# Performance work log

Measured on AMD Instinct MI355X. Metric: run time of the kernel, lower is better.

The kernel has to match this reference:

```python
import math
import jax, jax.numpy as jnp
import numpy as np


def _gelu(x):
    return jax.nn.gelu(x, approximate=False)


def _bilinear_sample(feat, gx, gy):
    """grid_sample, mode=bilinear, padding=border, align_corners=True.
    feat: [B,C,H,W]; gx,gy: [B,M] in [-1,1]. Returns [B,M,C]."""
    B, C, H, W = feat.shape
    x = jnp.clip((gx + 1.0) * 0.5 * (W - 1), 0.0, W - 1)
    y = jnp.clip((gy + 1.0) * 0.5 * (H - 1), 0.0, H - 1)
    x0 = jnp.floor(x); y0 = jnp.floor(y)
    wx = (x - x0)[..., None]; wy = (y - y0)[..., None]
    x0i = x0.astype(jnp.int32); y0i = y0.astype(jnp.int32)
    x1i = jnp.minimum(x0i + 1, W - 1); y1i = jnp.minimum(y0i + 1, H - 1)
    ft = jnp.transpose(feat, (0, 2, 3, 1))  # [B,H,W,C]
    gather = jax.vmap(lambda f, yi, xi: f[yi, xi])
    v00 = gather(ft, y0i, x0i); v01 = gather(ft, y0i, x1i)
    v10 = gather(ft, y1i, x0i); v11 = gather(ft, y1i, x1i)
    return (v00 * (1 - wx) * (1 - wy) + v01 * wx * (1 - wy)
            + v10 * (1 - wx) * wy + v11 * wx * wy)


def _layernorm(x, w, b, eps=1e-5):
    m = jnp.mean(x, -1, keepdims=True)
    v = jnp.var(x, -1, keepdims=True)
    return (x - m) / jnp.sqrt(v + eps) * w + b


def _gfb(h, f_next, ph_w, ph_b, gate, w1, b1, w2, b2, ln_w, ln_b):
    g = jax.nn.sigmoid(gate)
    fused = f_next + g * (h @ ph_w + ph_b)
    fused = _gelu(fused @ w1 + b1) @ w2 + b2
    return _layernorm(fused, ln_w, ln_b)


def _forward(img, feat_s8, feat_s16, coarse_flow, query_coords,
             pp_w1, pp_b1, pp_w2, pp_b2, p8_w, p8_b, p16_w, p16_b,
             f1_ph_w, f1_ph_b, f1_gate, f1_w1, f1_b1, f1_w2, f1_b2, f1_ln_w, f1_ln_b,
             f2_ph_w, f2_ph_b, f2_gate, f2_w1, f2_b1, f2_w2, f2_b2, f2_ln_w, f2_ln_b,
             h_w1, h_b1, h_w2, h_b2, h_w3, h_b3):
    B, _, H, W = img.shape
    N = query_coords.shape[1]
    k = 5; half = k // 2
    H8, W8 = coarse_flow.shape[2], coarse_flow.shape[3]
    # normalized grid at query points (x,y)
    gx = 2.0 * query_coords[..., 0] / (W - 1) - 1.0
    gy = 2.0 * query_coords[..., 1] / (H - 1) - 1.0
    coarse_q = _bilinear_sample(coarse_flow, gx, gy)  # [B,N,2]
    coarse_q = coarse_q * jnp.array([W / W8, H / H8], coarse_q.dtype)
    # local k x k RGB patches
    offs = jnp.arange(-half, half + 1, dtype=img.dtype)
    oy, ox = jnp.meshgrid(offs, offs, indexing='ij')
    og = jnp.stack([ox.reshape(-1), oy.reshape(-1)], -1)  # [k*k,2]
    ce = query_coords[:, :, None, :] + og                # [B,N,kk,2]
    pgx = (2.0 * ce[..., 0] / (W - 1) - 1.0).reshape(B, -1)
    pgy = (2.0 * ce[..., 1] / (H - 1) - 1.0).reshape(B, -1)
    patches = _bilinear_sample(img, pgx, pgy).reshape(B, N, k * k * 3)
    f_local = _gelu(patches @ pp_w1 + pp_b1) @ pp_w2 + pp_b2
    f8 = _bilinear_sample(feat_s8, gx, gy) @ p8_w + p8_b
    f16 = _bilinear_sample(feat_s16, gx, gy) @ p16_w + p16_b
    D = f_local.shape[-1]
    h = f_local.reshape(B * N, D)
    h = _gfb(h, f8.reshape(B * N, D), f1_ph_w, f1_ph_b, f1_gate,
             f1_w1, f1_b1, f1_w2, f1_b2, f1_ln_w, f1_ln_b)
    h = _gfb(h, f16.reshape(B * N, D), f2_ph_w, f2_ph_b, f2_gate,
             f2_w1, f2_b1, f2_w2, f2_b2, f2_ln_w, f2_ln_b)
    # relative-in-cell coords + sinusoidal PE (6 bands)
    qx = query_coords[..., 0] / (W / W8)
    qy = query_coords[..., 1] / (H / H8)
    local = jnp.stack([(qx - jnp.round(qx)) * 2.0, (qy - jnp.round(qy)) * 2.0], -1)
    freqs = (2.0 ** jnp.arange(6, dtype=local.dtype)) * math.pi
    xf = local[..., None] * freqs                        # [B,N,2,6]
    enc = jnp.concatenate([jnp.sin(xf), jnp.cos(xf)], -1).reshape(B, N, 24)
    pe = jnp.concatenate([local, enc], -1).reshape(B * N, 26)
    coarse_flat = coarse_q.reshape(B * N, 2)
    mi = jnp.concatenate([h, pe, coarse_flat], -1)       # [B*N, 156]
    delta = _gelu(_gelu(mi @ h_w1 + h_b1) @ h_w2 + h_b2) @ h_w3 + h_b3
    return (coarse_flat + delta).reshape(B, N, 2)


def setup_inputs() -> dict:
    key = jax.random.key(0)
    ks = jax.random.split(key, 40)
    B, H, W = 2, 384, 512
    H8, W8, H16, W16 = 48, 64, 24, 32
    N, D, k = 65536, 128, 5
    pf = 3 * k * k
    def p(i, shape):
        return jax.random.normal(ks[i], shape, jnp.float32) * 0.05
    return {
        'img': jax.random.uniform(ks[0], (B, 3, H, W), jnp.float32),
        'feat_s8': jax.random.normal(ks[1], (B, D, H8, W8), jnp.float32),
        'feat_s16': jax.random.normal(ks[2], (B, D, H16, W16), jnp.float32),
        'coarse_flow': jax.random.normal(ks[3], (B, 2, H8, W8), jnp.float32),
        'query_coords': jax.random.uniform(ks[4], (B, N, 2), jnp.float32)
                        * jnp.array([W - 1.0, H - 1.0], jnp.float32),
        'pp_w1': p(5, (pf, D)), 'pp_b1': p(6, (D,)),
        'pp_w2': p(7, (D, D)), 'pp_b2': p(8, (D,)),
        'p8_w': p(9, (D, D)), 'p8_b': p(10, (D,)),
        'p16_w': p(11, (D, D)), 'p16_b': p(12, (D,)),
        'f1_ph_w': p(13, (D, D)), 'f1_ph_b': p(14, (D,)), 'f1_gate': p(15, (D,)),
        'f1_w1': p(16, (D, 2 * D)), 'f1_b1': p(17, (2 * D,)),
        'f1_w2': p(18, (2 * D, D)), 'f1_b2': p(19, (D,)),
        'f1_ln_w': 1.0 + p(20, (D,)), 'f1_ln_b': p(21, (D,)),
        'f2_ph_w': p(22, (D, D)), 'f2_ph_b': p(23, (D,)), 'f2_gate': p(24, (D,)),
        'f2_w1': p(25, (D, 2 * D)), 'f2_b1': p(26, (2 * D,)),
        'f2_w2': p(27, (2 * D, D)), 'f2_b2': p(28, (D,)),
        'f2_ln_w': 1.0 + p(29, (D,)), 'f2_ln_b': p(30, (D,)),
        'h_w1': p(31, (D + 26 + 2, 128)), 'h_b1': p(32, (128,)),
        'h_w2': p(33, (128, 64)), 'h_b2': p(34, (64,)),
        'h_w3': p(35, (64, 2)), 'h_b3': p(36, (2,)),
    }


def reference(img, feat_s8, feat_s16, coarse_flow, query_coords,
              pp_w1, pp_b1, pp_w2, pp_b2, p8_w, p8_b, p16_w, p16_b,
              f1_ph_w, f1_ph_b, f1_gate, f1_w1, f1_b1, f1_w2, f1_b2, f1_ln_w, f1_ln_b,
              f2_ph_w, f2_ph_b, f2_gate, f2_w1, f2_b1, f2_w2, f2_b2, f2_ln_w, f2_ln_b,
              h_w1, h_b1, h_w2, h_b2, h_w3, h_b3):
    return _forward(img, feat_s8, feat_s16, coarse_flow, query_coords,
                    pp_w1, pp_b1, pp_w2, pp_b2, p8_w, p8_b, p16_w, p16_b,
                    f1_ph_w, f1_ph_b, f1_gate, f1_w1, f1_b1, f1_w2, f1_b2, f1_ln_w, f1_ln_b,
                    f2_ph_w, f2_ph_b, f2_gate, f2_w1, f2_b1, f2_w2, f2_b2, f2_ln_w, f2_ln_b,
                    h_w1, h_b1, h_w2, h_b2, h_w3, h_b3)
```

## Files before the change

kernel.cpp:

```cpp
#include <hip/hip_runtime.h>
#include <math.h>

#define NT 256
#define MB 32
#define MTOT 131072
#define IMG_H 384
#define IMG_W 512
#define H8 48
#define W8 64
#define H16 24
#define W16 32

typedef _Float16 half8_t __attribute__((ext_vector_type(8)));
typedef float f32x4_t __attribute__((ext_vector_type(4)));
typedef unsigned short u16;

#define PW_PP1   0
#define PW_PP2   12288
#define PW_P8    28672
#define PW_P16   45056
#define PW_F1PH  61440
#define PW_F1W1  77824
#define PW_F1W2  110592
#define PW_F2PH  143360
#define PW_F2W1  159744
#define PW_F2W2  192512
#define PW_HW1   225280
#define PW_HW2   245760
#define PW_END   253952
#define FT8_OFF  PW_END
#define FT8_CNT  (2*H8*W8*128)
#define FT16_OFF (FT8_OFF + FT8_CNT)

__device__ __forceinline__ u16 tohalf(float v) {
  return __builtin_bit_cast(u16, (_Float16)v);
}
__device__ __forceinline__ float geluf(float x) {
  float x2 = x * x;
  float t = x * fmaf(x2, 0.0713548162726f, 1.5957691216057308f);
  float e = __expf(-t);
  return x * __builtin_amdgcn_rcpf(1.0f + e);
}
__device__ __forceinline__ float sigm(float x) {
  return __builtin_amdgcn_rcpf(1.0f + __expf(-x));
}

__device__ __forceinline__ float bilin_plane(const float* __restrict__ plane,
                                             int Wd, int Hd, float x, float y) {
  x = fminf(fmaxf(x, 0.f), (float)(Wd - 1));
  y = fminf(fmaxf(y, 0.f), (float)(Hd - 1));
  float x0f = floorf(x), y0f = floorf(y);
  int x0 = (int)x0f, y0 = (int)y0f;
  int x1 = min(x0 + 1, Wd - 1), y1 = min(y0 + 1, Hd - 1);
  float wx = x - x0f, wy = y - y0f;
  const float* r0 = plane + y0 * Wd;
  const float* r1 = plane + y1 * Wd;
  float v00 = r0[x0], v01 = r0[x1], v10 = r1[x0], v11 = r1[x1];
  float top = v00 + wx * (v01 - v00);
  float bot = v10 + wx * (v11 - v10);
  return top + wy * (bot - top);
}

__device__ __forceinline__ void featSample(const u16* __restrict__ ft, int Wd, int Hd,
                                           float x, float y, u16* dstRow, int i16) {
  x = fminf(fmaxf(x, 0.f), (float)(Wd - 1));
  y = fminf(fmaxf(y, 0.f), (float)(Hd - 1));
  float x0f = floorf(x), y0f = floorf(y);
  int x0 = (int)x0f, y0 = (int)y0f;
  int x1 = min(x0 + 1, Wd - 1), y1 = min(y0 + 1, Hd - 1);
  float wx = x - x0f, wy = y - y0f;
  half8_t v00 = *reinterpret_cast<const half8_t*>(ft + (y0 * Wd + x0) * 128 + i16 * 8);
  half8_t v01 = *reinterpret_cast<const half8_t*>(ft + (y0 * Wd + x1) * 128 + i16 * 8);
  half8_t v10 = *reinterpret_cast<const half8_t*>(ft + (y1 * Wd + x0) * 128 + i16 * 8);
  half8_t v11 = *reinterpret_cast<const half8_t*>(ft + (y1 * Wd + x1) * 128 + i16 * 8);
  half8_t r;
#pragma unroll
  for (int j = 0; j < 8; ++j) {
    float top = (float)v00[j] + wx * ((float)v01[j] - (float)v00[j]);
    float bot = (float)v10[j] + wx * ((float)v11[j] - (float)v10[j]);
    r[j] = (_Float16)(top + wy * (bot - top));
  }
  *reinterpret_cast<half8_t*>(dstRow + i16 * 8) = r;
}

template <int NTW, int KT, int SPLITKT, int ACT>
__device__ __forceinline__ void mmv(
    const u16* __restrict__ wpk,
    const u16* aA, int strA, const u16* aB, int strB,
    const float* __restrict__ bias, const float* __restrict__ gate,
    u16* oA, int ostrA, u16* oB, int ostrB, int oSplitNt) {
  const int tid = threadIdx.x;
  const int lane = tid & 63;
  const int w = tid >> 6;
  const int l15 = lane & 15;
  const int g = lane >> 4;
  f32x4_t acc[NTW][2];
#pragma unroll
  for (int i = 0; i < NTW; ++i) {
    acc[i][0] = (f32x4_t){0.f, 0.f, 0.f, 0.f};
    acc[i][1] = (f32x4_t){0.f, 0.f, 0.f, 0.f};
  }
#pragma unroll
  for (int kt = 0; kt < KT; ++kt) {
    const u16* ab = (kt < SPLITKT) ? (aA + kt * 32) : (aB + (kt - SPLITKT) * 32);
    const int str = (kt < SPLITKT) ? strA : strB;
    half8_t af0 = *reinterpret_cast<const half8_t*>(ab + l15 * str + g * 8);
    half8_t af1 = *reinterpret_cast<const half8_t*>(ab + (16 + l15) * str + g * 8);
#pragma unroll
    for (int i = 0; i < NTW; ++i) {
      const int nt = w + (i << 2);
      half8_t bf = *reinterpret_cast<const half8_t*>(wpk + ((nt * KT + kt) * 64 + lane) * 8);
      acc[i][0] = __builtin_amdgcn_mfma_f32_16x16x32_f16(af0, bf, acc[i][0], 0, 0, 0);
      acc[i][1] = __builtin_amdgcn_mfma_f32_16x16x32_f16(af1, bf, acc[i][1], 0, 0, 0);
    }
  }
#pragma unroll
  for (int i = 0; i < NTW; ++i) {
    const int nt = w + (i << 2);
    const int colg = (nt << 4) + l15;
    float bv = bias[colg];
    float sg = 0.f;
    if (ACT == 2) sg = sigm(gate[colg]);
    u16* ob; int colB, ostr;
    if (nt < oSplitNt) { ob = oA; colB = colg; ostr = ostrA; }
    else { ob = oB; colB = colg - (oSplitNt << 4); ostr = ostrB; }
#pragma unroll
    for (int mt = 0; mt < 2; ++mt) {
#pragma unroll
      for (int r = 0; r < 4; ++r) {
        const int row = (mt << 4) + (g << 2) + r;
        float v = acc[i][mt][r] + bv;
        if (ACT == 1) v = geluf(v);
        if (ACT == 2) {
          _Float16 old = __builtin_bit_cast(_Float16, ob[row * ostr + colB]);
          v = (float)old + sg * v;
        }
        ob[row * ostr + colB] = tohalf(v);
      }
    }
  }
}

__device__ __forceinline__ void lnorm(const u16* src, u16* dst,
                                      const float* __restrict__ lw,
                                      const float* __restrict__ lb) {
  const int tid = threadIdx.x;
  int q = tid >> 3, s = tid & 7;
  const u16* rp = src + q * 136 + s * 16;
  float xs[16];
  float sum = 0.f, sum2 = 0.f;
#pragma unroll
  for (int c8 = 0; c8 < 2; ++c8) {
    half8_t v = *reinterpret_cast<const half8_t*>(rp + c8 * 8);
#pragma unroll
    for (int j = 0; j < 8; ++j) {
      float x = (float)v[j];
      xs[c8 * 8 + j] = x; sum += x; sum2 += x * x;
    }
  }
  sum += __shfl_xor(sum, 1); sum2 += __shfl_xor(sum2, 1);
  sum += __shfl_xor(sum, 2); sum2 += __shfl_xor(sum2, 2);
  sum += __shfl_xor(sum, 4); sum2 += __shfl_xor(sum2, 4);
  float mean = sum * 0.0078125f;
  float var = sum2 * 0.0078125f - mean * mean;
  float rstd = rsqrtf(var + 1e-5f);
  u16* op = dst + q * 168 + s * 16;
#pragma unroll
  for (int c8 = 0; c8 < 2; ++c8) {
    half8_t r;
#pragma unroll
    for (int j = 0; j < 8; ++j) {
      int c = s * 16 + c8 * 8 + j;
      r[j] = (_Float16)((xs[c8 * 8 + j] - mean) * rstd * lw[c] + lb[c]);
    }
    *reinterpret_cast<half8_t*>(op + c8 * 8) = r;
  }
}

struct PackArgs { const float* src[12]; u16* dst; };

__global__ void pack_weights(PackArgs a) {
  const int KTs[12]   = {3, 4, 4, 4, 4, 4, 8, 4, 4, 8, 5, 4};
  const int Ks[12]    = {75, 128, 128, 128, 128, 128, 256, 128, 128, 256, 156, 128};
  const int Ns[12]    = {128, 128, 128, 128, 128, 256, 128, 128, 256, 128, 128, 64};
  const int bases[13] = {0, 12288, 28672, 45056, 61440, 77824, 110592, 143360,
                         159744, 192512, 225280, 245760, 253952};
  int stride = gridDim.x * blockDim.x;
  for (int i = blockIdx.x * blockDim.x + threadIdx.x; i < PW_END; i += stride) {
    int s = 0;
    while (i >= bases[s + 1]) ++s;
    int rem = i - bases[s];
    int e = rem & 511, lane = e >> 3, j = e & 7;
    int ntkt = rem >> 9;
    int kt = ntkt % KTs[s], nt = ntkt / KTs[s];
    int k = kt * 32 + ((lane >> 4) << 3) + j;
    int col = (nt << 4) + (lane & 15);
    float v = (k < Ks[s]) ? a.src[s][k * Ns[s] + col] : 0.f;
    a.dst[i] = tohalf(v);
  }
}

__global__ void cvt_cl_f16(const float* __restrict__ src, u16* __restrict__ dst,
                           int Hd, int Wd) {
  int total = 2 * 128 * Hd * Wd;
  int stride = gridDim.x * blockDim.x;
  for (int i = blockIdx.x * blockDim.x + threadIdx.x; i < total; i += stride) {
    int x = i % Wd;
    int t = i / Wd;
    int y = t % Hd; t /= Hd;
    int c = t % 128;
    int b = t / 128;
    dst[((b * Hd + y) * Wd + x) * 128 + c] = tohalf(src[i]);
  }
}

struct KParams {
  const float *img, *coarse_flow, *qc;
  const u16 *wpk, *ft8, *ft16;
  const float *pp_b1, *pp_b2, *p8_b, *p16_b;
  const float *f1_ph_b, *f1_gate, *f1_b1, *f1_b2, *f1_ln_w, *f1_ln_b;
  const float *f2_ph_b, *f2_gate, *f2_b1, *f2_b2, *f2_ln_w, *f2_ln_b;
  const float *h_b1, *h_b2, *h_w3, *h_b3;
  float* out;
};

__global__ __launch_bounds__(NT, 4) void ifd_mfma(KParams P) {
  __shared__ __align__(16) u16 smem[14080];
  __shared__ float qcL[64];
  __shared__ float cb[64];
  u16* ab0 = smem;
  u16* ab1 = smem + 4352;
  u16* hb  = smem + 8704;

  const int tid = threadIdx.x;
  const int m0 = blockIdx.x * MB;

  if (tid < 64) qcL[tid] = P.qc[m0 * 2 + tid];
  __syncthreads();

  for (int i = tid; i < MB * 96; i += NT) {
    int q = i / 96, c = i - q * 96;
    u16 val = 0;
    if (c < 75) {
      int m = m0 + q, b = m >> 16;
      float qx = qcL[2 * q], qy = qcL[2 * q + 1];
      int p = c / 3, ch = c - p * 3;
      int iy = p / 5, ix = p - iy * 5;
      const float* plane = P.img + (b * 3 + ch) * (IMG_H * IMG_W);
      val = tohalf(bilin_plane(plane, IMG_W, IMG_H,
                               qx + (float)(ix - 2), qy + (float)(iy - 2)));
    }
    ab0[q * 136 + c] = val;
  }
  for (int i = tid; i < MB * 40; i += NT) {
    int q = i / 40, c = i - q * 40;
    int m = m0 + q, b = m >> 16;
    float qx = qcL[2 * q], qy = qcL[2 * q + 1];
    float val = 0.f;
    if (c < 26) {
      float qx8 = qx * 0.125f, qy8 = qy * 0.125f;
      float lx = (qx8 - rintf(qx8)) * 2.f, ly = (qy8 - rintf(qy8)) * 2.f;
      if (c < 2) val = c ? ly : lx;
      else {
        int k = c - 2;
        int dim = k / 12, tt = k - dim * 12;
        int band = tt % 6, iscos = tt / 6;
        float loc = dim ? ly : lx;
        float ang = loc * 3.14159265358979323846f * (float)(1 << band);
        val = iscos ? __cosf(ang) : __sinf(ang);
      }
    } else if (c < 28) {
      int o = c - 26;
      float x8 = qx * (63.f / 511.f), y8 = qy * (47.f / 383.f);
      float cv = 8.f * bilin_plane(P.coarse_flow + (b * 2 + o) * (H8 * W8), W8, H8, x8, y8);
      cb[q * 2 + o] = cv;
      val = cv;
    }
    hb[q * 168 + 128 + c] = tohalf(val);
  }
  __syncthreads();

  mmv<2, 3, 3, 1>(P.wpk + PW_PP1, ab0, 136, ab0, 136, P.pp_b1, nullptr,
                  ab1, 136, ab1, 136, 16);
  __syncthreads();
  mmv<2, 4, 4, 0>(P.wpk + PW_PP2, ab1, 136, ab1, 136, P.pp_b2, nullptr,
                  hb, 168, hb, 168, 16);
  for (int i = tid; i < MB * 16; i += NT) {
    int q = i >> 4, i16 = i & 15;
    int m = m0 + q, b = m >> 16;
    float x = qcL[2 * q] * (63.f / 511.f), y = qcL[2 * q + 1] * (47.f / 383.f);
    featSample(P.ft8 + b * (H8 * W8 * 128), W8, H8, x, y, ab0 + q * 136, i16);
  }
  __syncthreads();
  mmv<2, 4, 4, 0>(P.wpk + PW_P8, ab0, 136, ab0, 136, P.p8_b, nullptr,
                  ab1, 136, ab1, 136, 16);
  __syncthreads();
  mmv<2, 4, 4, 2>(P.wpk + PW_F1PH, hb, 168, hb, 168, P.f1_ph_b, P.f1_gate,
                  ab1, 136, ab1, 136, 16);
  __syncthreads();
  mmv<4, 4, 4, 1>(P.wpk + PW_F1W1, ab1, 136, ab1, 136, P.f1_b1, nullptr,
                  ab0, 136, hb, 168, 8);
  __syncthreads();
  mmv<2, 8, 4, 0>(P.wpk + PW_F1W2, ab0, 136, hb, 168, P.f1_b2, nullptr,
                  ab1, 136, ab1, 136, 16);
  __syncthreads();
  lnorm(ab1, hb, P.f1_ln_w, P.f1_ln_b);
  for (int i = tid; i < MB * 16; i += NT) {
    int q = i >> 4, i16 = i & 15;
    int m = m0 + q, b = m >> 16;
    float x = qcL[2 * q] * (31.f / 511.f), y = qcL[2 * q + 1] * (23.f / 383.f);
    featSample(P.ft16 + b * (H16 * W16 * 128), W16, H16, x, y, ab0 + q * 136, i16);
  }
  __syncthreads();
  mmv<2, 4, 4, 0>(P.wpk + PW_P16, ab0, 136, ab0, 136, P.p16_b, nullptr,
                  ab1, 136, ab1, 136, 16);
  __syncthreads();
  mmv<2, 4, 4, 2>(P.wpk + PW_F2PH, hb, 168, hb, 168, P.f2_ph_b, P.f2_gate,
                  ab1, 136, ab1, 136, 16);
  __syncthreads();
  mmv<4, 4, 4, 1>(P.wpk + PW_F2W1, ab1, 136, ab1, 136, P.f2_b1, nullptr,
                  ab0, 136, hb, 168, 8);
  __syncthreads();
  mmv<2, 8, 4, 0>(P.wpk + PW_F2W2, ab0, 136, hb, 168, P.f2_b2, nullptr,
                  ab1, 136, ab1, 136, 16);
  __syncthreads();
  lnorm(ab1, hb, P.f2_ln_w, P.f2_ln_b);
  __syncthreads();
  mmv<2, 5, 5, 1>(P.wpk + PW_HW1, hb, 168, hb, 168, P.h_b1, nullptr,
                  ab1, 136, ab1, 136, 16);
  __syncthreads();
  mmv<1, 4, 4, 1>(P.wpk + PW_HW2, ab1, 136, ab1, 136, P.h_b2, nullptr,
                  ab0, 136, ab0, 136, 16);
  __syncthreads();
  if (tid < 64) {
    int q = tid >> 1, o = tid & 1;
    float acc = P.h_b3[o];
    const u16* rp = ab0 + q * 136;
#pragma unroll
    for (int c8 = 0; c8 < 8; ++c8) {
      half8_t v = *reinterpret_cast<const half8_t*>(rp + c8 * 8);
#pragma unroll
      for (int j = 0; j < 8; ++j) acc += (float)v[j] * P.h_w3[(c8 * 8 + j) * 2 + o];
    }
    P.out[(m0 + q) * 2 + o] = cb[q * 2 + o] + acc;
  }
}

extern "C" void kernel_launch(void* const* d_in, const int* in_sizes, int n_in,
                              void* d_out, int out_size, void* d_ws, size_t ws_size,
                              hipStream_t stream) {
  u16* wp = (u16*)d_ws;

  PackArgs pa;
  pa.src[0]  = (const float*)d_in[5];
  pa.src[1]  = (const float*)d_in[7];
  pa.src[2]  = (const float*)d_in[9];
  pa.src[3]  = (const float*)d_in[11];
  pa.src[4]  = (const float*)d_in[13];
  pa.src[5]  = (const float*)d_in[16];
  pa.src[6]  = (const float*)d_in[18];
  pa.src[7]  = (const float*)d_in[22];
  pa.src[8]  = (const float*)d_in[25];
  pa.src[9]  = (const float*)d_in[27];
  pa.src[10] = (const float*)d_in[31];
  pa.src[11] = (const float*)d_in[33];
  pa.dst = wp;
  pack_weights<<<512, 256, 0, stream>>>(pa);
  cvt_cl_f16<<<1024, 256, 0, stream>>>((const float*)d_in[1], wp + FT8_OFF, H8, W8);
  cvt_cl_f16<<<256, 256, 0, stream>>>((const float*)d_in[2], wp + FT16_OFF, H16, W16);

  KParams P;
  P.img = (const float*)d_in[0];
  P.coarse_flow = (const float*)d_in[3];
  P.qc = (const float*)d_in[4];
  P.wpk = wp; P.ft8 = wp + FT8_OFF; P.ft16 = wp + FT16_OFF;
  P.pp_b1 = (const float*)d_in[6];  P.pp_b2 = (const float*)d_in[8];
  P.p8_b = (const float*)d_in[10];  P.p16_b = (const float*)d_in[12];
  P.f1_ph_b = (const float*)d_in[14]; P.f1_gate = (const float*)d_in[15];
  P.f1_b1 = (const float*)d_in[17]; P.f1_b2 = (const float*)d_in[19];
  P.f1_ln_w = (const float*)d_in[20]; P.f1_ln_b = (const float*)d_in[21];
  P.f2_ph_b = (const float*)d_in[23]; P.f2_gate = (const float*)d_in[24];
  P.f2_b1 = (const float*)d_in[26]; P.f2_b2 = (const float*)d_in[28];
  P.f2_ln_w = (const float*)d_in[29]; P.f2_ln_b = (const float*)d_in[30];
  P.h_b1 = (const float*)d_in[32]; P.h_b2 = (const float*)d_in[34];
  P.h_w3 = (const float*)d_in[35]; P.h_b3 = (const float*)d_in[36];
  P.out = (float*)d_out;

  ifd_mfma<<<MTOT / MB, NT, 0, stream>>>(P);
}
```

Baseline: 205.1 us.

## Fold gated projections into concatenated-K GEMMs and vectorize MFMA epilogue stores

The sigmoid gate and the two projection matmuls per fusion block are folded algebraically into one K=256 GEMM over the concatenated [feat, h] inputs, with the gated bias precomputed by a small kernel. This removes two GEMM stages, two barriers and the read-modify-write epilogue. The MFMA operands are swapped so each lane holds four consecutive output columns, which allows half4 stores and vector bias loads. Launch bounds are raised to 5 blocks per CU, which may cause register spills.

```diff
diff --git a/kernel.cpp b/kernel.cpp
--- a/kernel.cpp
+++ b/kernel.cpp
@@ -12,25 +12,26 @@
 #define W16 32
 
 typedef _Float16 half8_t __attribute__((ext_vector_type(8)));
+typedef _Float16 half4_t __attribute__((ext_vector_type(4)));
 typedef float f32x4_t __attribute__((ext_vector_type(4)));
 typedef unsigned short u16;
 
-#define PW_PP1   0
-#define PW_PP2   12288
-#define PW_P8    28672
-#define PW_P16   45056
-#define PW_F1PH  61440
-#define PW_F1W1  77824
-#define PW_F1W2  110592
-#define PW_F2PH  143360
-#define PW_F2W1  159744
-#define PW_F2W2  192512
-#define PW_HW1   225280
-#define PW_HW2   245760
-#define PW_END   253952
-#define FT8_OFF  PW_END
-#define FT8_CNT  (2*H8*W8*128)
-#define FT16_OFF (FT8_OFF + FT8_CNT)
+#define PW_PP1    0
+#define PW_PP2    12288
+#define PW_P8CAT  28672
+#define PW_P16CAT 61440
+#define PW_F1W1   94208
+#define PW_F1W2   126976
+#define PW_F2W1   159744
+#define PW_F2W2   192512
+#define PW_HW1    225280
+#define PW_HW2    245760
+#define PW_END    253952
+#define FT8_OFF   PW_END
+#define FT8_CNT   (2*H8*W8*128)
+#define FT16_OFF  (FT8_OFF + FT8_CNT)
+#define FT16_CNT  (2*H16*W16*128)
+#define FB_OFF    (FT16_OFF + FT16_CNT)
 
 __device__ __forceinline__ u16 tohalf(float v) {
   return __builtin_bit_cast(u16, (_Float16)v);
@@ -40,9 +41,6 @@
   float t = x * fmaf(x2, 0.0713548162726f, 1.5957691216057308f);
   float e = __expf(-t);
   return x * __builtin_amdgcn_rcpf(1.0f + e);
-}
-__device__ __forceinline__ float sigm(float x) {
-  return __builtin_amdgcn_rcpf(1.0f + __expf(-x));
 }
 
 __device__ __forceinline__ float bilin_plane(const float* __restrict__ plane,
@@ -87,7 +85,7 @@
 __device__ __forceinline__ void mmv(
     const u16* __restrict__ wpk,
     const u16* aA, int strA, const u16* aB, int strB,
-    const float* __restrict__ bias, const float* __restrict__ gate,
+    const float* __restrict__ bias,
     u16* oA, int ostrA, u16* oB, int ostrB, int oSplitNt) {
   const int tid = threadIdx.x;
   const int lane = tid & 63;
@@ -110,33 +108,29 @@
     for (int i = 0; i < NTW; ++i) {
       const int nt = w + (i << 2);
       half8_t bf = *reinterpret_cast<const half8_t*>(wpk + ((nt * KT + kt) * 64 + lane) * 8);
-      acc[i][0] = __builtin_amdgcn_mfma_f32_16x16x32_f16(af0, bf, acc[i][0], 0, 0, 0);
-      acc[i][1] = __builtin_amdgcn_mfma_f32_16x16x32_f16(af1, bf, acc[i][1], 0, 0, 0);
+      acc[i][0] = __builtin_amdgcn_mfma_f32_16x16x32_f16(bf, af0, acc[i][0], 0, 0, 0);
+      acc[i][1] = __builtin_amdgcn_mfma_f32_16x16x32_f16(bf, af1, acc[i][1], 0, 0, 0);
     }
   }
 #pragma unroll
   for (int i = 0; i < NTW; ++i) {
     const int nt = w + (i << 2);
-    const int colg = (nt << 4) + l15;
-    float bv = bias[colg];
-    float sg = 0.f;
-    if (ACT == 2) sg = sigm(gate[colg]);
+    const int colg = nt << 4;
+    f32x4_t bv = *reinterpret_cast<const f32x4_t*>(bias + colg + (g << 2));
     u16* ob; int colB, ostr;
     if (nt < oSplitNt) { ob = oA; colB = colg; ostr = ostrA; }
     else { ob = oB; colB = colg - (oSplitNt << 4); ostr = ostrB; }
 #pragma unroll
     for (int mt = 0; mt < 2; ++mt) {
+      const int row = (mt << 4) + l15;
+      half4_t hv;
 #pragma unroll
       for (int r = 0; r < 4; ++r) {
-        const int row = (mt << 4) + (g << 2) + r;
-        float v = acc[i][mt][r] + bv;
+        float v = acc[i][mt][r] + bv[r];
         if (ACT == 1) v = geluf(v);
-        if (ACT == 2) {
-          _Float16 old = __builtin_bit_cast(_Float16, ob[row * ostr + colB]);
-          v = (float)old + sg * v;
-        }
-        ob[row * ostr + colB] = tohalf(v);
+        hv[r] = (_Float16)v;
       }
+      *reinterpret_cast<half4_t*>(ob + row * ostr + colB + (g << 2)) = hv;
     }
   }
 }
@@ -177,13 +171,17 @@
   }
 }
 
-struct PackArgs { const float* src[12]; u16* dst; };
+struct PackArgs {
+  const float *pp_w1, *pp_w2, *p8_w, *f1_ph_w, *f1_gate, *p16_w, *f2_ph_w, *f2_gate;
+  const float *f1_w1, *f1_w2, *f2_w1, *f2_w2, *h_w1, *h_w2;
+  u16* dst;
+};
 
 __global__ void pack_weights(PackArgs a) {
-  const int KTs[12]   = {3, 4, 4, 4, 4, 4, 8, 4, 4, 8, 5, 4};
-  const int Ks[12]    = {75, 128, 128, 128, 128, 128, 256, 128, 128, 256, 156, 128};
-  const int Ns[12]    = {128, 128, 128, 128, 128, 256, 128, 128, 256, 128, 128, 64};
-  const int bases[13] = {0, 12288, 28672, 45056, 61440, 77824, 110592, 143360,
+  const int KTs[10]   = {3, 4, 8, 8, 4, 8, 4, 8, 5, 4};
+  const int Ks[10]    = {75, 128, 256, 256, 128, 256, 128, 256, 156, 128};
+  const int Ns[10]    = {128, 128, 128, 128, 256, 128, 256, 128, 128, 64};
+  const int bases[11] = {0, 12288, 28672, 61440, 94208, 126976,
                          159744, 192512, 225280, 245760, 253952};
   int stride = gridDim.x * blockDim.x;
   for (int i = blockIdx.x * blockDim.x + threadIdx.x; i < PW_END; i += stride) {
@@ -195,8 +193,37 @@
     int kt = ntkt % KTs[s], nt = ntkt / KTs[s];
     int k = kt * 32 + ((lane >> 4) << 3) + j;
     int col = (nt << 4) + (lane & 15);
-    float v = (k < Ks[s]) ? a.src[s][k * Ns[s] + col] : 0.f;
+    float v = 0.f;
+    if (k < Ks[s]) {
+      switch (s) {
+        case 0: v = a.pp_w1[k * 128 + col]; break;
+        case 1: v = a.pp_w2[k * 128 + col]; break;
+        case 2: v = (k < 128) ? a.p8_w[k * 128 + col]
+                              : a.f1_ph_w[(k - 128) * 128 + col] /
+                                    (1.f + expf(-a.f1_gate[col])); break;
+        case 3: v = (k < 128) ? a.p16_w[k * 128 + col]
+                              : a.f2_ph_w[(k - 128) * 128 + col] /
+                                    (1.f + expf(-a.f2_gate[col])); break;
+        case 4: v = a.f1_w1[k * 256 + col]; break;
+        case 5: v = a.f1_w2[k * 128 + col]; break;
+        case 6: v = a.f2_w1[k * 256 + col]; break;
+        case 7: v = a.f2_w2[k * 128 + col]; break;
+        case 8: v = a.h_w1[k * 128 + col]; break;
+        case 9: v = a.h_w2[k * 64 + col]; break;
+      }
+    }
     a.dst[i] = tohalf(v);
+  }
+}
+
+__global__ void fuse_bias(const float* __restrict__ p8_b, const float* __restrict__ f1_ph_b,
+                          const float* __restrict__ f1_gate,
+                          const float* __restrict__ p16_b, const float* __restrict__ f2_ph_b,
+                          const float* __restrict__ f2_gate, float* __restrict__ fb) {
+  int t = threadIdx.x;
+  if (t < 128) {
+    fb[t] = p8_b[t] + f1_ph_b[t] / (1.f + expf(-f1_gate[t]));
+    fb[128 + t] = p16_b[t] + f2_ph_b[t] / (1.f + expf(-f2_gate[t]));
   }
 }
 
@@ -217,14 +244,15 @@
 struct KParams {
   const float *img, *coarse_flow, *qc;
   const u16 *wpk, *ft8, *ft16;
-  const float *pp_b1, *pp_b2, *p8_b, *p16_b;
-  const float *f1_ph_b, *f1_gate, *f1_b1, *f1_b2, *f1_ln_w, *f1_ln_b;
-  const float *f2_ph_b, *f2_gate, *f2_b1, *f2_b2, *f2_ln_w, *f2_ln_b;
+  const float *fb;
+  const float *pp_b1, *pp_b2;
+  const float *f1_b1, *f1_b2, *f1_ln_w, *f1_ln_b;
+  const float *f2_b1, *f2_b2, *f2_ln_w, *f2_ln_b;
   const float *h_b1, *h_b2, *h_w3, *h_b3;
   float* out;
 };
 
-__global__ __launch_bounds__(NT, 4) void ifd_mfma(KParams P) {
+__global__ __launch_bounds__(NT, 5) void ifd_mfma(KParams P) {
   __shared__ __align__(16) u16 smem[14080];
   __shared__ float qcL[64];
   __shared__ float cb[64];
@@ -280,10 +308,10 @@
   }
   __syncthreads();
 
-  mmv<2, 3, 3, 1>(P.wpk + PW_PP1, ab0, 136, ab0, 136, P.pp_b1, nullptr,
-                  ab1, 136, ab1, 136, 16);
-  __syncthreads();
-  mmv<2, 4, 4, 0>(P.wpk + PW_PP2, ab1, 136, ab1, 136, P.pp_b2, nullptr,
+  mmv<2, 3, 3, 1>(P.wpk + PW_PP1, ab0, 136, ab0, 136, P.pp_b1,
+                  ab1, 136, ab1, 136, 16);
+  __syncthreads();
+  mmv<2, 4, 4, 0>(P.wpk + PW_PP2, ab1, 136, ab1, 136, P.pp_b2,
                   hb, 168, hb, 168, 16);
   for (int i = tid; i < MB * 16; i += NT) {
     int q = i >> 4, i16 = i & 15;
@@ -292,16 +320,13 @@
     featSample(P.ft8 + b * (H8 * W8 * 128), W8, H8, x, y, ab0 + q * 136, i16);
   }
   __syncthreads();
-  mmv<2, 4, 4, 0>(P.wpk + PW_P8, ab0, 136, ab0, 136, P.p8_b, nullptr,
-                  ab1, 136, ab1, 136, 16);
-  __syncthreads();
-  mmv<2, 4, 4, 2>(P.wpk + PW_F1PH, hb, 168, hb, 168, P.f1_ph_b, P.f1_gate,
-                  ab1, 136, ab1, 136, 16);
-  __syncthreads();
-  mmv<4, 4, 4, 1>(P.wpk + PW_F1W1, ab1, 136, ab1, 136, P.f1_b1, nullptr,
+  mmv<2, 8, 4, 0>(P.wpk + PW_P8CAT, ab0, 136, hb, 168, P.fb,
+                  ab1, 136, ab1, 136, 16);
+  __syncthreads();
+  mmv<4, 4, 4, 1>(P.wpk + PW_F1W1, ab1, 136, ab1, 136, P.f1_b1,
                   ab0, 136, hb, 168, 8);
   __syncthreads();
-  mmv<2, 8, 4, 0>(P.wpk + PW_F1W2, ab0, 136, hb, 168, P.f1_b2, nullptr,
+  mmv<2, 8, 4, 0>(P.wpk + PW_F1W2, ab0, 136, hb, 168, P.f1_b2,
                   ab1, 136, ab1, 136, 16);
   __syncthreads();
   lnorm(ab1, hb, P.f1_ln_w, P.f1_ln_b);
@@ -312,24 +337,21 @@
     featSample(P.ft16 + b * (H16 * W16 * 128), W16, H16, x, y, ab0 + q * 136, i16);
   }
   __syncthreads();
-  mmv<2, 4, 4, 0>(P.wpk + PW_P16, ab0, 136, ab0, 136, P.p16_b, nullptr,
-                  ab1, 136, ab1, 136, 16);
-  __syncthreads();
-  mmv<2, 4, 4, 2>(P.wpk + PW_F2PH, hb, 168, hb, 168, P.f2_ph_b, P.f2_gate,
-                  ab1, 136, ab1, 136, 16);
-  __syncthreads();
-  mmv<4, 4, 4, 1>(P.wpk + PW_F2W1, ab1, 136, ab1, 136, P.f2_b1, nullptr,
+  mmv<2, 8, 4, 0>(P.wpk + PW_P16CAT, ab0, 136, hb, 168, P.fb + 128,
+                  ab1, 136, ab1, 136, 16);
+  __syncthreads();
+  mmv<4, 4, 4, 1>(P.wpk + PW_F2W1, ab1, 136, ab1, 136, P.f2_b1,
                   ab0, 136, hb, 168, 8);
   __syncthreads();
-  mmv<2, 8, 4, 0>(P.wpk + PW_F2W2, ab0, 136, hb, 168, P.f2_b2, nullptr,
+  mmv<2, 8, 4, 0>(P.wpk + PW_F2W2, ab0, 136, hb, 168, P.f2_b2,
                   ab1, 136, ab1, 136, 16);
   __syncthreads();
   lnorm(ab1, hb, P.f2_ln_w, P.f2_ln_b);
   __syncthreads();
-  mmv<2, 5, 5, 1>(P.wpk + PW_HW1, hb, 168, hb, 168, P.h_b1, nullptr,
-                  ab1, 136, ab1, 136, 16);
-  __syncthreads();
-  mmv<1, 4, 4, 1>(P.wpk + PW_HW2, ab1, 136, ab1, 136, P.h_b2, nullptr,
+  mmv<2, 5, 5, 1>(P.wpk + PW_HW1, hb, 168, hb, 168, P.h_b1,
+                  ab1, 136, ab1, 136, 16);
+  __syncthreads();
+  mmv<1, 4, 4, 1>(P.wpk + PW_HW2, ab1, 136, ab1, 136, P.h_b2,
                   ab0, 136, ab0, 136, 16);
   __syncthreads();
   if (tid < 64) {
@@ -350,22 +372,28 @@
                               void* d_out, int out_size, void* d_ws, size_t ws_size,
                               hipStream_t stream) {
   u16* wp = (u16*)d_ws;
+  float* fb = (float*)(wp + FB_OFF);
 
   PackArgs pa;
-  pa.src[0]  = (const float*)d_in[5];
-  pa.src[1]  = (const float*)d_in[7];
-  pa.src[2]  = (const float*)d_in[9];
-  pa.src[3]  = (const float*)d_in[11];
-  pa.src[4]  = (const float*)d_in[13];
-  pa.src[5]  = (const float*)d_in[16];
-  pa.src[6]  = (const float*)d_in[18];
-  pa.src[7]  = (const float*)d_in[22];
-  pa.src[8]  = (const float*)d_in[25];
-  pa.src[9]  = (const float*)d_in[27];
-  pa.src[10] = (const float*)d_in[31];
-  pa.src[11] = (const float*)d_in[33];
+  pa.pp_w1  = (const float*)d_in[5];
+  pa.pp_w2  = (const float*)d_in[7];
+  pa.p8_w   = (const float*)d_in[9];
+  pa.p16_w  = (const float*)d_in[11];
+  pa.f1_ph_w = (const float*)d_in[13];
+  pa.f1_gate = (const float*)d_in[15];
+  pa.f1_w1  = (const float*)d_in[16];
+  pa.f1_w2  = (const float*)d_in[18];
+  pa.f2_ph_w = (const float*)d_in[22];
+  pa.f2_gate = (const float*)d_in[24];
+  pa.f2_w1  = (const float*)d_in[25];
+  pa.f2_w2  = (const float*)d_in[27];
+  pa.h_w1   = (const float*)d_in[31];
+  pa.h_w2   = (const float*)d_in[33];
   pa.dst = wp;
   pack_weights<<<512, 256, 0, stream>>>(pa);
+  fuse_bias<<<1, 128, 0, stream>>>((const float*)d_in[10], (const float*)d_in[14],
+                                   (const float*)d_in[15], (const float*)d_in[12],
+                                   (const float*)d_in[23], (const float*)d_in[24], fb);
   cvt_cl_f16<<<1024, 256, 0, stream>>>((const float*)d_in[1], wp + FT8_OFF, H8, W8);
   cvt_cl_f16<<<256, 256, 0, stream>>>((const float*)d_in[2], wp + FT16_OFF, H16, W16);
 
@@ -374,12 +402,10 @@
   P.coarse_flow = (const float*)d_in[3];
   P.qc = (const float*)d_in[4];
   P.wpk = wp; P.ft8 = wp + FT8_OFF; P.ft16 = wp + FT16_OFF;
+  P.fb = fb;
   P.pp_b1 = (const float*)d_in[6];  P.pp_b2 = (const float*)d_in[8];
-  P.p8_b = (const float*)d_in[10];  P.p16_b = (const float*)d_in[12];
-  P.f1_ph_b = (const float*)d_in[14]; P.f1_gate = (const float*)d_in[15];
   P.f1_b1 = (const float*)d_in[17]; P.f1_b2 = (const float*)d_in[19];
   P.f1_ln_w = (const float*)d_in[20]; P.f1_ln_b = (const float*)d_in[21];
-  P.f2_ph_b = (const float*)d_in[23]; P.f2_gate = (const float*)d_in[24];
   P.f2_b1 = (const float*)d_in[26]; P.f2_b2 = (const float*)d_in[28];
   P.f2_ln_w = (const float*)d_in[29]; P.f2_ln_b = (const float*)d_in[30];
   P.h_b1 = (const float*)d_in[32]; P.h_b2 = (const float*)d_in[34];
```

New measurement: 243.4 us. 1.19x slower.
